# Optimization experiments

Measured on AMD Instinct MI355X. Metric: run time of the kernel, lower is better.

Reference implementation:

```python
import jax, jax.numpy as jnp
import numpy as np

B, D, C, N = 8, 49, 512, 12
BN_EPS = 1e-5
SCALE = (C // 2) ** -0.5


def bn_train(x, axes):
    # training-mode batchnorm, gamma=1 beta=0 (per bn_init / default init)
    m = jnp.mean(x, axis=axes, keepdims=True)
    v = jnp.var(x, axis=axes, keepdims=True)
    return (x - m) * jax.lax.rsqrt(v + BN_EPS)


def l2norm(x):
    n = jnp.linalg.norm(x, axis=-1, keepdims=True)
    return x / jnp.maximum(n, 1e-12)


def cross_attn(y, xkv, wq, bq, wk, bk, wv, bv):
    q = y @ wq + bq
    k = xkv @ wk + bk
    v = xkv @ wv + bv
    a = jax.nn.softmax(jnp.einsum('...ik,...jk->...ij', q, k) * SCALE, axis=-1)
    return a @ v


def _gnn_layer(xv, ed, wa, wb, we, wu, wv):
    # incidence-matrix einsums reduce to repeat (end-gather) / tile (start-gather)
    res = xv
    agg = jnp.repeat(xv @ wa, N, axis=1) + jnp.tile(xv @ wb, (1, N, 1)) + ed @ we
    ed = ed + jax.nn.relu(bn_train(agg, (0, 2)))
    e = jax.nn.sigmoid(ed).reshape(-1, N, N, C)
    e = jax.nn.softmax(e, axis=2).reshape(-1, N * N, C)
    uj = jnp.tile(xv @ wv, (1, N, 1))
    msg = (e * uj).reshape(-1, N, N, C).sum(axis=2) / N  # scatter via end.T
    xv = jax.nn.relu(res + bn_train(xv @ wu + msg, (0, 2)))
    return xv, ed


def setup_inputs() -> dict:
    ks = iter(jax.random.split(jax.random.key(0), 64))

    def nrm(shape, scale=0.02):
        return jax.random.normal(next(ks), shape, dtype=jnp.float32) * scale

    g = float(np.sqrt(2.0 / C))
    inp = {'x': jax.random.normal(next(ks), (B, D, C), dtype=jnp.float32)}
    inp['Wc'] = nrm((N, C, C))
    inp['bc'] = nrm((N, C), 0.01)
    for p in ('fam', 'arm'):
        inp[p + '_wq'] = nrm((C, C // 2))
        inp[p + '_bq'] = nrm((C // 2,), 0.01)
        inp[p + '_wk'] = nrm((C, C // 2))
        inp[p + '_bk'] = nrm((C // 2,), 0.01)
        inp[p + '_wv'] = nrm((C, C))
        inp[p + '_bv'] = nrm((C,), 0.01)
    inp['ep_w'] = nrm((C, C))
    inp['ep_b'] = nrm((C,), 0.01)
    for nm in ('g_wa1', 'g_wb1', 'g_we1', 'g_wu1', 'g_wv1',
               'g_wa2', 'g_wb2', 'g_we2', 'g_wu2', 'g_wv2'):
        inp[nm] = nrm((C, C), g)
    inp['sc'] = nrm((N, C), float(np.sqrt(6.0 / (N + C))))
    inp['efc_w'] = nrm((C, 4), float(np.sqrt(6.0 / (C + 4))))
    inp['efc_b'] = nrm((4,), 0.01)
    return inp


def reference(x, Wc, bc,
              fam_wq, fam_bq, fam_wk, fam_bk, fam_wv, fam_bv,
              arm_wq, arm_bq, arm_wk, arm_bk, arm_wv, arm_bv,
              ep_w, ep_b,
              g_wa1, g_wb1, g_we1, g_wu1, g_wv1,
              g_wa2, g_wb2, g_we2, g_wu2, g_wv2,
              sc, efc_w, efc_b):
    b = x.shape[0]
    # per-class LinearBlocks (fc -> BN -> ReLU), vectorized over classes
    h = jnp.einsum('bdc,nco->bndo', x, Wc) + bc[None, :, None, :]
    f_u = jax.nn.relu(bn_train(h, (0, 2)))          # (b, N, D, C)
    f_v = f_u.mean(axis=2)                           # (b, N, C)
    # GEM edge extractor
    gf = jnp.broadcast_to(x[:, None], (b, N, D, C))
    feat = cross_attn(f_u, gf, fam_wq, fam_bq, fam_wk, fam_bk, fam_wv, fam_bv)
    feat_end = jnp.repeat(feat, N, axis=1)           # (b, N*N, D, C): edge (i,j) -> node i
    feat_start = jnp.tile(feat, (1, N, 1, 1))        # edge (i,j) -> node j
    feat = cross_attn(feat_start, feat_end, arm_wq, arm_bq, arm_wk, arm_bk, arm_wv, arm_bv)
    f_e = bn_train(feat @ ep_w + ep_b, (0, 2, 3)).mean(axis=2)  # (b, N*N, C)
    # cosine-similarity adjacency mask (detached), digraph-normalized
    si = l2norm(jax.lax.stop_gradient(f_v))
    adj = jnp.einsum('bik,bjk->bij', si, si)
    dis = jnp.sum(adj, axis=-1) ** -0.5
    mask = (adj * dis[:, :, None] * dis[:, None, :]).reshape(b, N * N, 1)
    f_e = f_e * mask
    # two GNN message-passing layers
    f_v, f_e = _gnn_layer(f_v, f_e, g_wa1, g_wb1, g_we1, g_wu1, g_wv1)
    f_v, f_e = _gnn_layer(f_v, f_e, g_wa2, g_wb2, g_we2, g_wu2, g_wv2)
    # cosine classifier + edge fc
    scn = l2norm(jax.nn.relu(sc))
    cl = jnp.sum(l2norm(f_v) * scn[None], axis=-1)   # (b, N)
    cl_edge = f_e @ efc_w + efc_b                    # (b, N*N, 4)
    return cl, cl_edge
```

## Files before the change

### kernel.cpp

```cpp
#include <hip/hip_runtime.h>
#include <math.h>

namespace {

constexpr int B = 8, D = 49, C = 512, N = 12, H = 256, E = 144;
constexpr int M_BD  = B * D;
constexpr int M_BND = B * N * D;
constexpr float BN_EPS = 1e-5f;
constexpr float ATT_SCALE = 0.0625f;

typedef __attribute__((ext_vector_type(4))) float  floatx4;
typedef __attribute__((ext_vector_type(8))) short  shortx8;

__device__ inline unsigned short f2bf(float f) {
  unsigned u = __float_as_uint(f);
  return (unsigned short)((u + 0x7fffu + ((u >> 16) & 1u)) >> 16);
}
__device__ inline float bf2f(unsigned short u) {
  return __uint_as_float(((unsigned)u) << 16);
}

__device__ inline void gload16(const unsigned short* g, unsigned short* l) {
  __builtin_amdgcn_global_load_lds(
      (const __attribute__((address_space(1))) void*)g,
      (__attribute__((address_space(3))) void*)l, 16, 0, 0);
}

struct TCJobs {
  const float* src[28];
  unsigned short* dst[28];
  int nn[28];
};

__global__ __launch_bounds__(256)
void tcast_k(TCJobs jobs,
             const float* __restrict__ x, unsigned short* __restrict__ xb,
             const float* __restrict__ awv, unsigned short* __restrict__ armwvb,
             const float* __restrict__ bk, const float* __restrict__ bv,
             const float* __restrict__ bq2, const float* __restrict__ bk2,
             const float* __restrict__ arm_bv, const float* __restrict__ epw,
             const float* __restrict__ epb,
             float* __restrict__ kvbias, float* __restrict__ qkvbias)
{
  const int z = blockIdx.z;
  const int tid = threadIdx.x;
  if (z == 28) {
    int idx = (blockIdx.y * 16 + blockIdx.x) * 256 + tid;
    const int n1 = M_BD * C / 8;
    const int n2 = n1 + C * C / 8;
    if (idx < n1) {
      int i8 = idx * 8;
      float4 a = *reinterpret_cast<const float4*>(x + i8);
      float4 b = *reinterpret_cast<const float4*>(x + i8 + 4);
      shortx8 o;
      o[0]=(short)f2bf(a.x); o[1]=(short)f2bf(a.y); o[2]=(short)f2bf(a.z); o[3]=(short)f2bf(a.w);
      o[4]=(short)f2bf(b.x); o[5]=(short)f2bf(b.y); o[6]=(short)f2bf(b.z); o[7]=(short)f2bf(b.w);
      *reinterpret_cast<shortx8*>(xb + i8) = o;
    } else if (idx < n2) {
      int i8 = (idx - n1) * 8;
      float4 a = *reinterpret_cast<const float4*>(awv + i8);
      float4 b = *reinterpret_cast<const float4*>(awv + i8 + 4);
      shortx8 o;
      o[0]=(short)f2bf(a.x); o[1]=(short)f2bf(a.y); o[2]=(short)f2bf(a.z); o[3]=(short)f2bf(a.w);
      o[4]=(short)f2bf(b.x); o[5]=(short)f2bf(b.y); o[6]=(short)f2bf(b.z); o[7]=(short)f2bf(b.w);
      *reinterpret_cast<shortx8*>(armwvb + i8) = o;
    } else if (idx >= 58112 && idx < 58624) {
      int c = idx - 58112;
      float s = epb[c];
      for (int k = 0; k < C; ++k) s = fmaf(arm_bv[k], epw[k * C + c], s);
      qkvbias[512 + c] = s;
    }
    if (idx < 256) { kvbias[idx] = bk[idx]; qkvbias[idx] = bq2[idx]; qkvbias[256 + idx] = bk2[idx]; }
    if (idx < 512) kvbias[256 + idx] = bv[idx];
    return;
  }
  const float* src = jobs.src[z];
  unsigned short* dst = jobs.dst[z];
  const int Nn = jobs.nn[z];
  const int tx = blockIdx.x, ty = blockIdx.y;
  if (tx * 32 >= Nn) return;
  __shared__ float t[32][33];
  const int lr = tid >> 5, lc = tid & 31;
#pragma unroll
  for (int p = 0; p < 4; ++p) {
    int k = ty * 32 + p * 8 + lr;
    t[p * 8 + lr][lc] = src[(long long)k * Nn + tx * 32 + lc];
  }
  __syncthreads();
#pragma unroll
  for (int p = 0; p < 4; ++p) {
    int n = tx * 32 + p * 8 + lr;
    dst[(long long)n * 512 + ty * 32 + lc] = f2bf(t[lc][p * 8 + lr]);
  }
}

__device__ __forceinline__
void gemm64_body(const void* __restrict__ Ain, const unsigned short* __restrict__ Bt,
                 const float* __restrict__ bp, float* __restrict__ co,
                 unsigned short* __restrict__ cb,
                 int M, int Nn, int K, int lda, int ldb, int ldc, int abf,
                 int bx, int by)
{
  const float* Af = abf ? nullptr : (const float*)Ain;
  const unsigned short* Ab = abf ? (const unsigned short*)Ain : nullptr;

  __shared__ short As[64 * 72];
  __shared__ short Bs[64 * 72];

  const int tid = threadIdx.x;
  const int row0 = bx * 64, col0 = by * 64;
  const int wid = tid >> 6, lane = tid & 63;
  const int wr = wid >> 1, wc = wid & 1;
  const int lr = lane & 15, lg = lane >> 4;

  floatx4 acc00 = {0.f,0.f,0.f,0.f}, acc01 = {0.f,0.f,0.f,0.f};
  floatx4 acc10 = {0.f,0.f,0.f,0.f}, acc11 = {0.f,0.f,0.f,0.f};

  const int r = tid >> 2, seg = tid & 3;
  const int gr = row0 + r, gn = col0 + r;
  short* aw = &As[r * 72 + seg * 16];
  short* bw = &Bs[r * 72 + seg * 16];
  const shortx8 zz = {0,0,0,0,0,0,0,0};

  for (int k0 = 0; k0 < K; k0 += 64) {
    shortx8 w0, w1;
    if (gr < M) {
      if (abf) {
        const shortx8* ap = reinterpret_cast<const shortx8*>(Ab + (long long)gr * lda + seg * 16 + k0);
        w0 = ap[0]; w1 = ap[1];
      } else {
        const float4* ap = reinterpret_cast<const float4*>(Af + (long long)gr * lda + seg * 16 + k0);
        float4 fa0 = ap[0], fa1 = ap[1], fa2 = ap[2], fa3 = ap[3];
        w0[0]=(short)f2bf(fa0.x); w0[1]=(short)f2bf(fa0.y); w0[2]=(short)f2bf(fa0.z); w0[3]=(short)f2bf(fa0.w);
        w0[4]=(short)f2bf(fa1.x); w0[5]=(short)f2bf(fa1.y); w0[6]=(short)f2bf(fa1.z); w0[7]=(short)f2bf(fa1.w);
        w1[0]=(short)f2bf(fa2.x); w1[1]=(short)f2bf(fa2.y); w1[2]=(short)f2bf(fa2.z); w1[3]=(short)f2bf(fa2.w);
        w1[4]=(short)f2bf(fa3.x); w1[5]=(short)f2bf(fa3.y); w1[6]=(short)f2bf(fa3.z); w1[7]=(short)f2bf(fa3.w);
      }
    } else { w0 = zz; w1 = zz; }
    const shortx8* bp8 = reinterpret_cast<const shortx8*>(Bt + (long long)gn * ldb + seg * 16 + k0);
    shortx8 b0v = bp8[0];
    shortx8 b1v = bp8[1];

    __syncthreads();
    *reinterpret_cast<shortx8*>(aw)     = w0;
    *reinterpret_cast<shortx8*>(aw + 8) = w1;
    *reinterpret_cast<shortx8*>(bw)     = b0v;
    *reinterpret_cast<shortx8*>(bw + 8) = b1v;
    __syncthreads();

#pragma unroll
    for (int kt = 0; kt < 2; ++kt) {
      shortx8 a0 = *reinterpret_cast<const shortx8*>(&As[(wr*32      + lr) * 72 + kt*32 + lg*8]);
      shortx8 a1 = *reinterpret_cast<const shortx8*>(&As[(wr*32 + 16 + lr) * 72 + kt*32 + lg*8]);
      shortx8 bb0 = *reinterpret_cast<const shortx8*>(&Bs[(wc*32      + lr) * 72 + kt*32 + lg*8]);
      shortx8 bb1 = *reinterpret_cast<const shortx8*>(&Bs[(wc*32 + 16 + lr) * 72 + kt*32 + lg*8]);
      acc00 = __builtin_amdgcn_mfma_f32_16x16x32_bf16(a0, bb0, acc00, 0, 0, 0);
      acc01 = __builtin_amdgcn_mfma_f32_16x16x32_bf16(a0, bb1, acc01, 0, 0, 0);
      acc10 = __builtin_amdgcn_mfma_f32_16x16x32_bf16(a1, bb0, acc10, 0, 0, 0);
      acc11 = __builtin_amdgcn_mfma_f32_16x16x32_bf16(a1, bb1, acc11, 0, 0, 0);
    }
  }

  const int colA = col0 + wc * 32 + lr;
  const int colB = colA + 16;
  const bool okA = colA < Nn, okB = colB < Nn;
  const float biasA = (bp && okA) ? bp[colA] : 0.f;
  const float biasB = (bp && okB) ? bp[colB] : 0.f;
  const int rb0 = row0 + wr * 32 + lg * 4;
  const int rb1 = rb0 + 16;
#pragma unroll
  for (int jj = 0; jj < 4; ++jj) {
    int ra = rb0 + jj, rb = rb1 + jj;
    float v00 = acc00[jj] + biasA, v01 = acc01[jj] + biasB;
    float v10 = acc10[jj] + biasA, v11 = acc11[jj] + biasB;
    if (ra < M) {
      if (co) { if (okA) co[(long long)ra * ldc + colA] = v00;
                if (okB) co[(long long)ra * ldc + colB] = v01; }
      if (cb) { if (okA) cb[(long long)ra * ldc + colA] = f2bf(v00);
                if (okB) cb[(long long)ra * ldc + colB] = f2bf(v01); }
    }
    if (rb < M) {
      if (co) { if (okA) co[(long long)rb * ldc + colA] = v10;
                if (okB) co[(long long)rb * ldc + colB] = v11; }
      if (cb) { if (okA) cb[(long long)rb * ldc + colA] = f2bf(v10);
                if (okB) cb[(long long)rb * ldc + colB] = f2bf(v11); }
    }
  }
}

__global__ __launch_bounds__(256)
void gemm_mfma(const void* __restrict__ Ain, const unsigned short* __restrict__ Bt,
               const float* __restrict__ bias, float* __restrict__ Co,
               unsigned short* __restrict__ Cb,
               int M, int Nn, int K, int lda, int ldb, int ldc, int abf,
               long long sA, long long sB, long long sBias, long long sC)
{
  const int z = blockIdx.z;
  const void* A = abf ? (const void*)((const unsigned short*)Ain + z * sA)
                      : (const void*)((const float*)Ain + z * sA);
  gemm64_body(A, Bt + z * sB, bias ? bias + z * sBias : nullptr,
              Co ? Co + z * sC : nullptr, Cb ? Cb + z * sC : nullptr,
              M, Nn, K, lda, ldb, ldc, abf, blockIdx.x, blockIdx.y);
}

struct GJob {
  const void* A; const unsigned short* B; const float* bias;
  float* Co; unsigned short* Cb;
  int M, Nn, K, lda, ldb, ldc, abf, tx;
};
struct GJobs { GJob j[3]; int ends[3]; int n; };

__global__ __launch_bounds__(256)
void gemm_jobs(GJobs js)
{
  const int bid = blockIdx.x;
#pragma unroll
  for (int q = 0; q < 3; ++q) {
    if (q < js.n && bid < js.ends[q]) {
      int start = q ? js.ends[q - 1] : 0;
      int local = bid - start;
      const GJob& J = js.j[q];
      gemm64_body(J.A, J.B, J.bias, J.Co, J.Cb,
                  J.M, J.Nn, J.K, J.lda, J.ldb, J.ldc, J.abf,
                  local % J.tx, local / J.tx);
      return;
    }
  }
}

__device__ __forceinline__
void g128_body(const unsigned short* __restrict__ Ab, const unsigned short* __restrict__ Bt,
               const float* __restrict__ bp, float* __restrict__ co,
               unsigned short* __restrict__ cb, float* __restrict__ psb, float* __restrict__ pqb,
               int M, int Nn, int K, int lda, int ldb, int ldc, int bx, int by)
{
  __shared__ unsigned short As[128 * 64];
  __shared__ unsigned short Bs[128 * 64];

  const int tid = threadIdx.x;
  const int row0 = bx * 128, col0 = by * 128;
  const int wid = tid >> 6, lane = tid & 63;
  const int wr = wid >> 1, wc = wid & 1;
  const int lr = lane & 15, lg = lane >> 4;

  floatx4 acc[4][4];
#pragma unroll
  for (int mf = 0; mf < 4; ++mf)
#pragma unroll
    for (int nf = 0; nf < 4; ++nf) acc[mf][nf] = floatx4{0.f,0.f,0.f,0.f};

  const int rsub = tid >> 3;
  const int csub = (tid & 7) * 8;

  for (int k0 = 0; k0 < K; k0 += 64) {
    __syncthreads();
#pragma unroll
    for (int it = 0; it < 4; ++it) {
      int r = it * 32 + rsub;
      gload16(Ab + (long long)(row0 + r) * lda + k0 + csub, As + it * 2048 + tid * 8);
      gload16(Bt + (long long)(col0 + r) * ldb + k0 + csub, Bs + it * 2048 + tid * 8);
    }
    __syncthreads();

#pragma unroll
    for (int kt = 0; kt < 2; ++kt) {
      shortx8 af[4], bf[4];
#pragma unroll
      for (int mf = 0; mf < 4; ++mf)
        af[mf] = *reinterpret_cast<const shortx8*>(&As[(wr*64 + mf*16 + lr) * 64 + kt*32 + lg*8]);
#pragma unroll
      for (int nf = 0; nf < 4; ++nf)
        bf[nf] = *reinterpret_cast<const shortx8*>(&Bs[(wc*64 + nf*16 + lr) * 64 + kt*32 + lg*8]);
#pragma unroll
      for (int mf = 0; mf < 4; ++mf)
#pragma unroll
        for (int nf = 0; nf < 4; ++nf)
          acc[mf][nf] = __builtin_amdgcn_mfma_f32_16x16x32_bf16(af[mf], bf[nf], acc[mf][nf], 0, 0, 0);
    }
  }

#pragma unroll
  for (int nf = 0; nf < 4; ++nf) {
    const int col = col0 + wc * 64 + nf * 16 + lr;
    if (col >= Nn) continue;
    const float bv = bp ? bp[col] : 0.f;
#pragma unroll
    for (int mf = 0; mf < 4; ++mf) {
      const int rbase = row0 + wr * 64 + mf * 16 + lg * 4;
#pragma unroll
      for (int jj = 0; jj < 4; ++jj) {
        int row = rbase + jj;
        if (row >= M) continue;
        float v = acc[mf][nf][jj] + bv;
        if (co) co[(long long)row * ldc + col] = v;
        if (cb) cb[(long long)row * ldc + col] = f2bf(v);
      }
    }
  }

  if (psb) {
    __syncthreads();
    float* sb = (float*)As;
    sb[tid] = 0.f;
    __syncthreads();
#pragma unroll
    for (int nf = 0; nf < 4; ++nf) {
      const int lcol = wc * 64 + nf * 16 + lr;
      const int col = col0 + lcol;
      float s = 0.f, q = 0.f;
      if (col < Nn) {
        const float bv = bp ? bp[col] : 0.f;
#pragma unroll
        for (int mf = 0; mf < 4; ++mf) {
          const int rbase = row0 + wr * 64 + mf * 16 + lg * 4;
#pragma unroll
          for (int jj = 0; jj < 4; ++jj) {
            if (rbase + jj < M) { float v = acc[mf][nf][jj] + bv; s += v; q += v * v; }
          }
        }
      }
      atomicAdd(&sb[lcol], s);
      atomicAdd(&sb[128 + lcol], q);
    }
    __syncthreads();
    if (tid < 128) {
      psb[col0 + tid] = sb[tid];
      pqb[col0 + tid] = sb[128 + tid];
    }
  }
}

__global__ __launch_bounds__(256)
void gemm128g(const unsigned short* __restrict__ Ab, const unsigned short* __restrict__ Bt,
              const float* __restrict__ bias, float* __restrict__ Co,
              unsigned short* __restrict__ Cb, float* __restrict__ ps, float* __restrict__ pq,
              int M, int Nn, int K, int lda, int ldb, int ldc,
              long long sA, long long sB, long long sBias, long long sC)
{
  const int z = blockIdx.z;
  long long so = ((long long)blockIdx.x * gridDim.z + z) * ldc;
  g128_body(Ab + z * sA, Bt + z * sB, bias ? bias + z * sBias : nullptr,
            Co ? Co + z * sC : nullptr, Cb ? Cb + z * sC : nullptr,
            ps ? ps + so : nullptr, pq ? pq + so : nullptr,
            M, Nn, K, lda, ldb, ldc, blockIdx.x, blockIdx.y);
}

__global__ __launch_bounds__(256)
void scgm_k(const unsigned short* __restrict__ qkvfe, float* __restrict__ Sc,
            float* __restrict__ Gm)
{
  const int bid = blockIdx.x;
  if (bid < 200) {
    int z = bid / 25, rem = bid % 25;
    g128_body(qkvfe + (long long)z * 588 * 1024, qkvfe + 256 + (long long)z * 588 * 1024,
              nullptr, Sc + (long long)z * 588 * 588, nullptr, nullptr, nullptr,
              588, 588, H, 1024, 1024, 588, rem % 5, rem / 5);
  } else {
    int z = bid - 200;
    const unsigned short* vp = qkvfe + 512 + (long long)z * 49 * 1024;
    gemm64_body(vp, vp, nullptr, Gm + (long long)z * 2401, nullptr,
                D, D, C, 1024, 1024, D, 1, 0, 0);
  }
}

__global__ __launch_bounds__(256)
void gnn_gemm_k(const unsigned short* __restrict__ feb, const unsigned short* __restrict__ wet,
                float* __restrict__ EW, const float* __restrict__ fv,
                const unsigned short* __restrict__ ABUVt, float* __restrict__ ABUV)
{
  const int bid = blockIdx.x;
  if (bid < 36) {
    g128_body(feb, wet, nullptr, EW, nullptr, nullptr, nullptr,
              B * E, C, C, C, C, C, bid % 9, bid / 9);
  } else {
    int local = bid - 36;
    gemm64_body(fv, ABUVt, nullptr, ABUV, nullptr,
                B * N, 2048, C, C, C, 2048, 0, local % 2, local / 2);
  }
}

__global__ __launch_bounds__(256)
void fu_fv(const unsigned short* __restrict__ hb, const float* __restrict__ ps,
           const float* __restrict__ pq, unsigned short* __restrict__ fub,
           float* __restrict__ fv)
{
  const int bid = blockIdx.x;
  const int b = bid / N, n = bid % N;
  const int c = blockIdx.y * 256 + threadIdx.x;
  const int idx = n * C + c;
  float s = 0.f, q = 0.f;
#pragma unroll
  for (int sl = 0; sl < 4; ++sl) { s += ps[sl * (N * C) + idx]; q += pq[sl * (N * C) + idx]; }
  float m = s / (float)M_BD;
  float rv = rsqrtf(q / (float)M_BD - m * m + BN_EPS);
  float acc = 0.f;
  for (int d = 0; d < D; ++d) {
    float v = bf2f(hb[((long long)n * M_BD + b * D + d) * C + c]);
    v = fmaxf((v - m) * rv, 0.f);
    fub[((long long)bid * D + d) * C + c] = f2bf(v);
    acc += v;
  }
  fv[(long long)bid * C + c] = acc * (1.0f / (float)D);
}

__global__ __launch_bounds__(256)
void softvxt_k(const float* __restrict__ Sf, unsigned short* __restrict__ Ppb,
               const unsigned short* __restrict__ kvx, unsigned short* __restrict__ vxtb,
               const float* __restrict__ fv, float* __restrict__ maskp)
{
  const int tid = threadIdx.x;
  if (blockIdx.x < 19) {
    int row = blockIdx.x * 256 + tid;
    if (row >= M_BND) return;
    const float* p = Sf + (long long)row * 49;
    float v[49];
    float m = -1e30f;
#pragma unroll
    for (int j = 0; j < 49; ++j) { v[j] = p[j] * ATT_SCALE; m = fmaxf(m, v[j]); }
    float s = 0.f;
#pragma unroll
    for (int j = 0; j < 49; ++j) { v[j] = __expf(v[j] - m); s += v[j]; }
    float inv = 1.f / s;
    unsigned short* o = Ppb + (long long)row * 64;
#pragma unroll
    for (int j = 0; j < 49; ++j) o[j] = f2bf(v[j] * inv);
#pragma unroll
    for (int j = 49; j < 64; ++j) o[j] = 0;
    return;
  }
  if (blockIdx.x < 83) {
    const int i = blockIdx.x - 19;
    const int b = i >> 3, cc = i & 7;
    __shared__ unsigned short t[49][65];
    for (int idx = tid; idx < 49 * 64; idx += 256) {
      int rr = idx >> 6, k = idx & 63;
      t[rr][k] = kvx[(long long)(b * 49 + rr) * 768 + 256 + cc * 64 + k];
    }
    __syncthreads();
    for (int idx = tid; idx < 64 * 64; idx += 256) {
      int n = idx >> 6, kk = idx & 63;
      vxtb[((long long)b * 512 + cc * 64 + n) * 64 + kk] = (kk < 49) ? t[kk][n] : (unsigned short)0;
    }
    return;
  }
  const int b = blockIdx.x - 83;
  __shared__ float fl[N][C];
  __shared__ float adj[N][N];
  __shared__ float nrm[N];
  __shared__ float dis[N];
  for (int idx = tid; idx < N * C; idx += 256)
    fl[idx / C][idx % C] = fv[(long long)b * N * C + idx];
  __syncthreads();
  if (tid < N * N) {
    int i = tid / N, j = tid % N;
    float s = 0.f;
    for (int k = 0; k < C; ++k) s += fl[i][k] * fl[j][k];
    adj[i][j] = s;
  }
  __syncthreads();
  if (tid < N) nrm[tid] = fmaxf(sqrtf(adj[tid][tid]), 1e-12f);
  __syncthreads();
  if (tid < N * N) {
    int i = tid / N, j = tid % N;
    adj[i][j] = adj[i][j] / (nrm[i] * nrm[j]);
  }
  __syncthreads();
  if (tid < N) {
    float s = 0.f;
    for (int j = 0; j < N; ++j) s += adj[tid][j];
    dis[tid] = rsqrtf(s);
  }
  __syncthreads();
  if (tid < N * N) {
    int i = tid / N, j = tid % N;
    maskp[b * E + tid] = adj[i][j] * dis[i] * dis[j];
  }
}

__global__ __launch_bounds__(256)
void edge_finish(const float* __restrict__ Sc, const float* __restrict__ G,
                 const unsigned short* __restrict__ qkvfe,
                 float* __restrict__ S1, float* __restrict__ eS)
{
  const int bid = blockIdx.x;
  const int b = bid / E, e = bid % E;
  const int i = e / N, j = e % N;
  const float* Scb = Sc + (long long)b * 588 * 588 + (long long)(j * 49) * 588 + i * 49;
  const float* Gp  = G + (long long)(b * N + i) * 2401;
  const unsigned short* Vp = qkvfe + (long long)(b * N + i) * D * 1024 + 512;

  __shared__ float aT[49][53];
  __shared__ float g[49][53];
  __shared__ unsigned short abT[64][72];
  __shared__ float ws[52];
  __shared__ float r0[4], r1[4];
  const int tid = threadIdx.x;
  const int wid = tid >> 6, lane = tid & 63;
  const int lr = lane & 15, lg = lane >> 4;

  for (int idx = tid; idx < 49 * 49; idx += 256) {
    int di = idx / 49, dj = idx - di * 49;
    aT[dj][di] = Scb[di * 588 + dj] * ATT_SCALE;
    g[di][dj] = Gp[idx];
  }
  __syncthreads();
  if (tid < D) {
    float m = -1e30f;
    for (int jj = 0; jj < D; ++jj) m = fmaxf(m, aT[jj][tid]);
    float s = 0.f;
    for (int jj = 0; jj < D; ++jj) { float ev = __expf(aT[jj][tid] - m); aT[jj][tid] = ev; s += ev; }
    float inv = 1.f / s;
    for (int jj = 0; jj < D; ++jj) aT[jj][tid] *= inv;
  }
  __syncthreads();
  for (int idx = tid; idx < 64 * 64; idx += 256) {
    int dj = idx >> 6, di = idx & 63;
    float v = (dj < D && di < D) ? aT[dj][di] : 0.f;
    abT[dj][di] = f2bf(v);
  }
  if (tid < D) {
    float s = 0.f;
    for (int di = 0; di < D; ++di) s += aT[tid][di];
    ws[tid] = s;
  }
  __syncthreads();

  floatx4 acc[4];
#pragma unroll
  for (int tk = 0; tk < 4; ++tk) acc[tk] = floatx4{0.f,0.f,0.f,0.f};
  shortx8 af0 = *reinterpret_cast<const shortx8*>(&abT[wid * 16 + lr][lg * 8]);
  shortx8 af1 = *reinterpret_cast<const shortx8*>(&abT[wid * 16 + lr][32 + lg * 8]);
#pragma unroll
  for (int tk = 0; tk < 4; ++tk) {
    shortx8 bf0v = *reinterpret_cast<const shortx8*>(&abT[tk * 16 + lr][lg * 8]);
    shortx8 bf1v = *reinterpret_cast<const shortx8*>(&abT[tk * 16 + lr][32 + lg * 8]);
    acc[tk] = __builtin_amdgcn_mfma_f32_16x16x32_bf16(af0, bf0v, acc[tk], 0, 0, 0);
    acc[tk] = __builtin_amdgcn_mfma_f32_16x16x32_bf16(af1, bf1v, acc[tk], 0, 0, 0);
  }
  float st2 = 0.f;
#pragma unroll
  for (int tk = 0; tk < 4; ++tk) {
    int kcol = tk * 16 + lr;
#pragma unroll
    for (int rg = 0; rg < 4; ++rg) {
      int jrow = wid * 16 + lg * 4 + rg;
      if (jrow < D && kcol < D) st2 = fmaf(acc[tk][rg], g[jrow][kcol], st2);
    }
  }

  const unsigned* Vp32 = reinterpret_cast<const unsigned*>(Vp);
  float s1a = 0.f, s1b = 0.f;
  for (int dk = 0; dk < D; ++dk) {
    unsigned u = Vp32[dk * 512 + tid];
    float w = ws[dk];
    s1a = fmaf(w, bf2f((unsigned short)(u & 0xffffu)), s1a);
    s1b = fmaf(w, bf2f((unsigned short)(u >> 16)), s1b);
  }
  S1[(long long)bid * C + 2 * tid]     = s1a;
  S1[(long long)bid * C + 2 * tid + 1] = s1b;
  float st = s1a + s1b;

  for (int off = 32; off; off >>= 1) { st += __shfl_down(st, off); st2 += __shfl_down(st2, off); }
  if (lane == 0) { r0[wid] = st; r1[wid] = st2; }
  __syncthreads();
  if (tid == 0) {
    eS[bid * 2 + 0] = r0[0] + r0[1] + r0[2] + r0[3];
    eS[bid * 2 + 1] = r1[0] + r1[1] + r1[2] + r1[3];
  }
}

__global__ __launch_bounds__(256)
void fe_k(const float* __restrict__ S1, const float* __restrict__ eS,
          const float* __restrict__ maskp, float* __restrict__ fe,
          unsigned short* __restrict__ feb)
{
  __shared__ float csh[3];
  long long idx0 = (long long)blockIdx.x * 256;
  long long be = idx0 / C;
  int e = (int)(be % E);
  if (threadIdx.x == 0) {
    float s = 0.f, q = 0.f;
    for (int b = 0; b < B; ++b) { s += eS[(b * E + e) * 2]; q += eS[(b * E + e) * 2 + 1]; }
    const float inv = 1.f / (float)(B * D * C);
    float m = s * inv;
    csh[0] = m;
    csh[1] = rsqrtf(q * inv - m * m + BN_EPS);
    csh[2] = maskp[be];
  }
  __syncthreads();
  long long idx = idx0 + threadIdx.x;
  float v = (S1[idx] * (1.0f / (float)D) - csh[0]) * csh[1] * csh[2];
  fe[idx] = v;
  feb[idx] = f2bf(v);
}

__global__ __launch_bounds__(256)
void agg_stats(const float* __restrict__ ABUV, const float* __restrict__ EW,
               float* __restrict__ mu_e, float* __restrict__ rs_e)
{
  const int e = blockIdx.x;
  const int i = e / N, j = e % N;
  const int tid = threadIdx.x;
  float s = 0.f, q = 0.f;
  for (int idx = tid; idx < B * C; idx += 256) {
    int b = idx >> 9, c = idx & 511;
    float v = ABUV[(long long)(b * N + i) * 2048 + c]
            + ABUV[(long long)(b * N + j) * 2048 + 512 + c]
            + EW[((long long)b * E + e) * C + c];
    s += v; q += v * v;
  }
  for (int off = 32; off; off >>= 1) { s += __shfl_down(s, off); q += __shfl_down(q, off); }
  __shared__ float r0[4], r1[4];
  int wid = tid >> 6, lane = tid & 63;
  if (lane == 0) { r0[wid] = s; r1[wid] = q; }
  __syncthreads();
  if (tid == 0) {
    float ss = r0[0] + r0[1] + r0[2] + r0[3];
    float qq = r1[0] + r1[1] + r1[2] + r1[3];
    float m = ss / (float)(B * C);
    mu_e[e] = m;
    rs_e[e] = rsqrtf(qq / (float)(B * C) - m * m + BN_EPS);
  }
}

__global__ __launch_bounds__(256)
void edmsg_k(float* __restrict__ fe, unsigned short* __restrict__ feb,
             const float* __restrict__ ABUV,
             const float* __restrict__ EW, const float* __restrict__ mu_e,
             const float* __restrict__ rs_e, float* __restrict__ pre,
             float* __restrict__ nps, float* __restrict__ npq)
{
  const int bid = blockIdx.x;
  const int b = bid / N, i = bid % N;
  const int tid = threadIdx.x;
  float ls = 0.f, lq = 0.f;
  for (int c = tid; c < C; c += 256) {
    float ai = ABUV[(long long)(b * N + i) * 2048 + c];
    float sv[N];
    float m = -1e30f;
#pragma unroll
    for (int jn = 0; jn < N; ++jn) {
      int e = i * N + jn;
      float v = ai + ABUV[(long long)(b * N + jn) * 2048 + 512 + c]
              + EW[((long long)b * E + e) * C + c];
      v = (v - mu_e[e]) * rs_e[e];
      long long fidx = ((long long)b * E + e) * C + c;
      float ed = fe[fidx] + fmaxf(v, 0.f);
      fe[fidx] = ed;
      feb[fidx] = f2bf(ed);
      float sg = 1.f / (1.f + __expf(-ed));
      sv[jn] = sg; m = fmaxf(m, sg);
    }
    float sum = 0.f;
#pragma unroll
    for (int jn = 0; jn < N; ++jn) { float ev = __expf(sv[jn] - m); sv[jn] = ev; sum += ev; }
    float acc = 0.f;
#pragma unroll
    for (int jn = 0; jn < N; ++jn)
      acc = fmaf(sv[jn], ABUV[(long long)(b * N + jn) * 2048 + 1536 + c], acc);
    acc /= (sum * (float)N);
    float pv = ABUV[(long long)bid * 2048 + 1024 + c] + acc;
    pre[(long long)bid * C + c] = pv;
    ls += pv; lq += pv * pv;
  }
  for (int off = 32; off; off >>= 1) { ls += __shfl_down(ls, off); lq += __shfl_down(lq, off); }
  __shared__ float r0[4], r1[4];
  int wid = tid >> 6, lane = tid & 63;
  if (lane == 0) { r0[wid] = ls; r1[wid] = lq; }
  __syncthreads();
  if (tid == 0) {
    nps[i * B + b] = r0[0] + r0[1] + r0[2] + r0[3];
    npq[i * B + b] = r1[0] + r1[1] + r1[2] + r1[3];
  }
}

__global__ void xv_update(float* __restrict__ xv, const float* __restrict__ pre,
                          const float* __restrict__ nps, const float* __restrict__ npq)
{
  long long idx = (long long)blockIdx.x * 256 + threadIdx.x;
  if (idx >= (long long)B * N * C) return;
  int i = (int)((idx / C) % N);
  float s = 0.f, q = 0.f;
#pragma unroll
  for (int bb = 0; bb < B; ++bb) { s += nps[i * B + bb]; q += npq[i * B + bb]; }
  float mu = s * (1.f / (float)(B * C));
  float rs = rsqrtf(q * (1.f / (float)(B * C)) - mu * mu + BN_EPS);
  float v = xv[idx] + (pre[idx] - mu) * rs;
  xv[idx] = fmaxf(v, 0.f);
}

__global__ __launch_bounds__(256)
void out_k(const float* __restrict__ xv, const float* __restrict__ sc,
           const float* __restrict__ ed, const float* __restrict__ w,
           const float* __restrict__ bias, float* __restrict__ out)
{
  const int bid = blockIdx.x;
  const int tid = threadIdx.x;
  int wid = tid >> 6, lane = tid & 63;
  if (bid < B * N) {
    const int b = bid / N, i = bid % N;
    float sxx = 0.f, sss = 0.f, sxs = 0.f;
    for (int c = tid; c < C; c += 256) {
      float xvv = xv[(long long)(b * N + i) * C + c];
      float scv = fmaxf(sc[i * C + c], 0.f);
      sxx += xvv * xvv; sss += scv * scv; sxs += xvv * scv;
    }
    for (int off = 32; off; off >>= 1) {
      sxx += __shfl_down(sxx, off);
      sss += __shfl_down(sss, off);
      sxs += __shfl_down(sxs, off);
    }
    __shared__ float r0[4], r1[4], r2[4];
    if (lane == 0) { r0[wid] = sxx; r1[wid] = sss; r2[wid] = sxs; }
    __syncthreads();
    if (tid == 0) {
      float a = r0[0] + r0[1] + r0[2] + r0[3];
      float s = r1[0] + r1[1] + r1[2] + r1[3];
      float p = r2[0] + r2[1] + r2[2] + r2[3];
      float nx = fmaxf(sqrtf(a), 1e-12f);
      float ns = fmaxf(sqrtf(s), 1e-12f);
      out[b * N + i] = p / (nx * ns);
    }
  } else {
    const int eb = bid - B * N;
    float a0 = 0, a1 = 0, a2 = 0, a3 = 0;
    for (int c = tid; c < C; c += 256) {
      float v = ed[(long long)eb * C + c];
      a0 = fmaf(v, w[c * 4 + 0], a0);
      a1 = fmaf(v, w[c * 4 + 1], a1);
      a2 = fmaf(v, w[c * 4 + 2], a2);
      a3 = fmaf(v, w[c * 4 + 3], a3);
    }
    for (int off = 32; off; off >>= 1) {
      a0 += __shfl_down(a0, off);
      a1 += __shfl_down(a1, off);
      a2 += __shfl_down(a2, off);
      a3 += __shfl_down(a3, off);
    }
    __shared__ float r[4][4];
    if (lane == 0) { r[wid][0] = a0; r[wid][1] = a1; r[wid][2] = a2; r[wid][3] = a3; }
    __syncthreads();
    if (tid < 4) {
      float s = r[0][tid] + r[1][tid] + r[2][tid] + r[3][tid];
      out[B * N + eb * 4 + tid] = s + bias[tid];
    }
  }
}

}

extern "C" void kernel_launch(void* const* d_in, const int* in_sizes, int n_in,
                              void* d_out, int out_size, void* d_ws, size_t ws_size,
                              hipStream_t stream)
{
  (void)in_sizes; (void)n_in; (void)out_size; (void)ws_size;
  const float* x      = (const float*)d_in[0];
  const float* Wc     = (const float*)d_in[1];
  const float* bc     = (const float*)d_in[2];
  const float* fam_wq = (const float*)d_in[3];
  const float* fam_bq = (const float*)d_in[4];
  const float* fam_wk = (const float*)d_in[5];
  const float* fam_bk = (const float*)d_in[6];
  const float* fam_wv = (const float*)d_in[7];
  const float* fam_bv = (const float*)d_in[8];
  const float* arm_wq = (const float*)d_in[9];
  const float* arm_bq = (const float*)d_in[10];
  const float* arm_wk = (const float*)d_in[11];
  const float* arm_bk = (const float*)d_in[12];
  const float* arm_wv = (const float*)d_in[13];
  const float* arm_bv = (const float*)d_in[14];
  const float* ep_w   = (const float*)d_in[15];
  const float* ep_b   = (const float*)d_in[16];
  const float* gw[10] = {
    (const float*)d_in[17], (const float*)d_in[18], (const float*)d_in[19],
    (const float*)d_in[20], (const float*)d_in[21],
    (const float*)d_in[22], (const float*)d_in[23], (const float*)d_in[24],
    (const float*)d_in[25], (const float*)d_in[26]};
  const float* sc     = (const float*)d_in[27];
  const float* efc_w  = (const float*)d_in[28];
  const float* efc_b  = (const float*)d_in[29];
  float* out = (float*)d_out;

  char* wsb = (char*)d_ws;
  size_t off = 0;
  auto allocf = [&](size_t n) { float* p = (float*)(wsb + off); off += ((n * 4 + 255) / 256) * 256; return p; };
  auto allocu = [&](size_t n) { unsigned short* p = (unsigned short*)(wsb + off); off += ((n * 2 + 255) / 256) * 256; return p; };

  float* Sc    = allocf(2766336);
  float* bnp_s = allocf(24576);
  float* bnp_q = allocf(24576);
  float* f_v   = allocf(49152);
  float* Sf    = allocf(230496);
  float* Gm    = allocf(230496);
  float* S1    = allocf(589824);
  float* fe    = allocf(589824);
  float* EW    = allocf(589824);
  float* eS    = allocf(2304);
  float* mask  = allocf(1152);
  float* ABUV  = allocf(196608);
  float* pre   = allocf(49152);
  float* mu_e  = allocf(144);
  float* rs_e  = allocf(144);
  float* nps   = allocf(96);
  float* npq   = allocf(96);
  float* kvbias  = allocf(768);
  float* qkvbias = allocf(1024);

  unsigned short* Wct    = allocu(3145728);
  unsigned short* famqt  = allocu(131072);
  unsigned short* kvwt   = allocu(393216);
  unsigned short* qkw2t  = allocu(524288);
  unsigned short* epwt   = allocu(262144);
  unsigned short* armwvb = allocu(262144);
  unsigned short* wet0   = allocu(262144);
  unsigned short* wet1   = allocu(262144);
  unsigned short* ABUVt0 = allocu(1048576);
  unsigned short* ABUVt1 = allocu(1048576);
  unsigned short* xb     = allocu(262144);
  unsigned short* hb     = allocu(2408448);
  unsigned short* fub    = allocu(2408448);
  unsigned short* q1b    = allocu(1204224);
  unsigned short* kxvx_b = allocu(350208);
  unsigned short* Ppb    = allocu(301056);
  unsigned short* vxtb   = allocu(262144);
  unsigned short* featb  = allocu(2424832);
  unsigned short* qkvfe  = allocu(4915200);
  unsigned short* feb    = allocu(589824);

  dim3 blk(256);

  TCJobs tj{};
  int jn = 0;
  for (int n = 0; n < 12; ++n) { tj.src[jn] = Wc + (size_t)n * C * C; tj.dst[jn] = Wct + (size_t)n * C * C; tj.nn[jn] = C; ++jn; }
  tj.src[jn] = fam_wq; tj.dst[jn] = famqt;             tj.nn[jn] = H; ++jn;
  tj.src[jn] = fam_wk; tj.dst[jn] = kvwt;              tj.nn[jn] = H; ++jn;
  tj.src[jn] = fam_wv; tj.dst[jn] = kvwt + 256 * 512;  tj.nn[jn] = C; ++jn;
  tj.src[jn] = arm_wq; tj.dst[jn] = qkw2t;             tj.nn[jn] = H; ++jn;
  tj.src[jn] = arm_wk; tj.dst[jn] = qkw2t + 256 * 512; tj.nn[jn] = H; ++jn;
  tj.src[jn] = ep_w;   tj.dst[jn] = epwt;              tj.nn[jn] = C; ++jn;
  tj.src[jn] = gw[2];  tj.dst[jn] = wet0;              tj.nn[jn] = C; ++jn;
  tj.src[jn] = gw[7];  tj.dst[jn] = wet1;              tj.nn[jn] = C; ++jn;
  tj.src[jn] = gw[0];  tj.dst[jn] = ABUVt0;               tj.nn[jn] = C; ++jn;
  tj.src[jn] = gw[1];  tj.dst[jn] = ABUVt0 + 1 * C * C;   tj.nn[jn] = C; ++jn;
  tj.src[jn] = gw[3];  tj.dst[jn] = ABUVt0 + 2 * C * C;   tj.nn[jn] = C; ++jn;
  tj.src[jn] = gw[4];  tj.dst[jn] = ABUVt0 + 3 * C * C;   tj.nn[jn] = C; ++jn;
  tj.src[jn] = gw[5];  tj.dst[jn] = ABUVt1;               tj.nn[jn] = C; ++jn;
  tj.src[jn] = gw[6];  tj.dst[jn] = ABUVt1 + 1 * C * C;   tj.nn[jn] = C; ++jn;
  tj.src[jn] = gw[8];  tj.dst[jn] = ABUVt1 + 2 * C * C;   tj.nn[jn] = C; ++jn;
  tj.src[jn] = gw[9];  tj.dst[jn] = ABUVt1 + 3 * C * C;   tj.nn[jn] = C; ++jn;
  tcast_k<<<dim3(16, 16, 29), blk, 0, stream>>>(tj, x, xb, arm_wv, armwvb,
      fam_bk, fam_bv, arm_bq, arm_bk, arm_bv, ep_w, ep_b, kvbias, qkvbias);

  gemm128g<<<dim3(4, 4, 12), blk, 0, stream>>>(xb, Wct, bc, nullptr, hb, bnp_s, bnp_q,
      M_BD, C, C, C, C, C, 0LL, (long long)C * C, (long long)C, (long long)M_BD * C);
  fu_fv<<<dim3(B * N, 2), blk, 0, stream>>>(hb, bnp_s, bnp_q, fub, f_v);

  {
    GJobs js{};
    js.j[0] = {fub,  famqt,  fam_bq, nullptr, q1b,            M_BND, H,   C, C, C, H,   1, 74};
    js.j[1] = {xb,   kvwt,   kvbias, nullptr, kxvx_b,         M_BD,  768, C, C, C, 768, 1, 7};
    js.j[2] = {epwt, armwvb, nullptr, nullptr, qkw2t + 512 * 512, C,  C,   C, C, C, C,   1, 8};
    js.ends[0] = 296; js.ends[1] = 380; js.ends[2] = 444; js.n = 3;
    gemm_jobs<<<dim3(444), blk, 0, stream>>>(js);
  }
  gemm_mfma<<<dim3(10, 1, 8), blk, 0, stream>>>(q1b, kxvx_b, nullptr, Sf, nullptr,
      588, 49, H, H, 768, 49, 1, 588LL * 256, 49LL * 768, 0LL, 588LL * 49);
  softvxt_k<<<dim3(91), blk, 0, stream>>>(Sf, Ppb, kxvx_b, vxtb, f_v, mask);
  gemm_mfma<<<dim3(10, 8, 8), blk, 0, stream>>>(Ppb, vxtb, nullptr, nullptr, featb,
      588, C, 64, 64, 64, C, 1, 588LL * 64, 512LL * 64, 0LL, 588LL * 512);

  gemm128g<<<dim3(37, 8, 1), blk, 0, stream>>>(featb, qkw2t, qkvbias, nullptr, qkvfe,
      nullptr, nullptr, M_BND, 1024, C, C, C, 1024, 0, 0, 0, 0);

  scgm_k<<<dim3(296), blk, 0, stream>>>(qkvfe, Sc, Gm);

  edge_finish<<<dim3(B * E), blk, 0, stream>>>(Sc, Gm, qkvfe, S1, eS);
  fe_k<<<dim3(2304), blk, 0, stream>>>(S1, eS, mask, fe, feb);

  for (int L = 0; L < 2; ++L) {
    const unsigned short* ABUVt = L ? ABUVt1 : ABUVt0;
    const unsigned short* wet   = L ? wet1 : wet0;
    gnn_gemm_k<<<dim3(100), blk, 0, stream>>>(feb, wet, EW, f_v, ABUVt, ABUV);
    agg_stats<<<dim3(E), blk, 0, stream>>>(ABUV, EW, mu_e, rs_e);
    edmsg_k<<<dim3(B * N), blk, 0, stream>>>(fe, feb, ABUV, EW, mu_e, rs_e, pre, nps, npq);
    xv_update<<<dim3((B * N * C + 255) / 256), blk, 0, stream>>>(f_v, pre, nps, npq);
  }

  out_k<<<dim3(B * N + B * E), blk, 0, stream>>>(f_v, sc, fe, efc_w, efc_b, out);
}
```

Measured before the change: 213.7 us.

## Regroup projection GEMMs, store attention scores in bf16, fuse final node update

Merges the per-class projection GEMM with the kv and ep-weight GEMMs into one launch, and gives the fam query projection its own launch, which cuts kernel count and regroups independent work. The arm-attention score matrix and the Gram matrix are now written and read as bf16 instead of fp32, halving that intermediate traffic. The second layer's xv_update is folded into out_k, which recomputes the batchnorm, residual and relu inline. The bf16 scores add rounding before softmax, and the fu_fv dependency now waits on a larger combined kernel.

```diff
diff --git a/kernel.cpp b/kernel.cpp
--- a/kernel.cpp
+++ b/kernel.cpp
@@ -203,31 +203,6 @@
               M, Nn, K, lda, ldb, ldc, abf, blockIdx.x, blockIdx.y);
 }
 
-struct GJob {
-  const void* A; const unsigned short* B; const float* bias;
-  float* Co; unsigned short* Cb;
-  int M, Nn, K, lda, ldb, ldc, abf, tx;
-};
-struct GJobs { GJob j[3]; int ends[3]; int n; };
-
-__global__ __launch_bounds__(256)
-void gemm_jobs(GJobs js)
-{
-  const int bid = blockIdx.x;
-#pragma unroll
-  for (int q = 0; q < 3; ++q) {
-    if (q < js.n && bid < js.ends[q]) {
-      int start = q ? js.ends[q - 1] : 0;
-      int local = bid - start;
-      const GJob& J = js.j[q];
-      gemm64_body(J.A, J.B, J.bias, J.Co, J.Cb,
-                  J.M, J.Nn, J.K, J.lda, J.ldb, J.ldc, J.abf,
-                  local % J.tx, local / J.tx);
-      return;
-    }
-  }
-}
-
 __device__ __forceinline__
 void g128_body(const unsigned short* __restrict__ Ab, const unsigned short* __restrict__ Bt,
                const float* __restrict__ bp, float* __restrict__ co,
@@ -346,36 +321,48 @@
 }
 
 __global__ __launch_bounds__(256)
-void scgm_k(const unsigned short* __restrict__ qkvfe, float* __restrict__ Sc,
-            float* __restrict__ Gm)
+void proj1_k(const unsigned short* __restrict__ xb, const unsigned short* __restrict__ Wct,
+             const float* __restrict__ bc, unsigned short* __restrict__ hb,
+             float* __restrict__ ps, float* __restrict__ pq,
+             const unsigned short* __restrict__ kvwt, const float* __restrict__ kvbias,
+             unsigned short* __restrict__ kxvx_b,
+             const unsigned short* __restrict__ epwt, const unsigned short* __restrict__ armwvb,
+             unsigned short* __restrict__ w2out)
+{
+  const int bid = blockIdx.x;
+  if (bid < 192) {
+    int z = bid >> 4, rem = bid & 15;
+    int bx = rem & 3, by = rem >> 2;
+    long long so = ((long long)bx * 12 + z) * C;
+    g128_body(xb, Wct + (long long)z * C * C, bc + (long long)z * C,
+              nullptr, hb + (long long)z * M_BD * C, ps + so, pq + so,
+              M_BD, C, C, C, C, C, bx, by);
+  } else if (bid < 276) {
+    int local = bid - 192;
+    gemm64_body(xb, kvwt, kvbias, nullptr, kxvx_b, M_BD, 768, C, C, C, 768, 1,
+                local % 7, local / 7);
+  } else {
+    int local = bid - 276;
+    gemm64_body(epwt, armwvb, nullptr, nullptr, w2out, C, C, C, C, C, C, 1,
+                local % 8, local / 8);
+  }
+}
+
+__global__ __launch_bounds__(256)
+void scgm_k(const unsigned short* __restrict__ qkvfe, unsigned short* __restrict__ Sc16,
+            unsigned short* __restrict__ Gm16)
 {
   const int bid = blockIdx.x;
   if (bid < 200) {
     int z = bid / 25, rem = bid % 25;
     g128_body(qkvfe + (long long)z * 588 * 1024, qkvfe + 256 + (long long)z * 588 * 1024,
-              nullptr, Sc + (long long)z * 588 * 588, nullptr, nullptr, nullptr,
+              nullptr, nullptr, Sc16 + (long long)z * 588 * 588, nullptr, nullptr,
               588, 588, H, 1024, 1024, 588, rem % 5, rem / 5);
   } else {
     int z = bid - 200;
     const unsigned short* vp = qkvfe + 512 + (long long)z * 49 * 1024;
-    gemm64_body(vp, vp, nullptr, Gm + (long long)z * 2401, nullptr,
+    gemm64_body(vp, vp, nullptr, nullptr, Gm16 + (long long)z * 2401,
                 D, D, C, 1024, 1024, D, 1, 0, 0);
-  }
-}
-
-__global__ __launch_bounds__(256)
-void gnn_gemm_k(const unsigned short* __restrict__ feb, const unsigned short* __restrict__ wet,
-                float* __restrict__ EW, const float* __restrict__ fv,
-                const unsigned short* __restrict__ ABUVt, float* __restrict__ ABUV)
-{
-  const int bid = blockIdx.x;
-  if (bid < 36) {
-    g128_body(feb, wet, nullptr, EW, nullptr, nullptr, nullptr,
-              B * E, C, C, C, C, C, bid % 9, bid / 9);
-  } else {
-    int local = bid - 36;
-    gemm64_body(fv, ABUVt, nullptr, ABUV, nullptr,
-                B * N, 2048, C, C, C, 2048, 0, local % 2, local / 2);
   }
 }
 
@@ -478,15 +465,15 @@
 }
 
 __global__ __launch_bounds__(256)
-void edge_finish(const float* __restrict__ Sc, const float* __restrict__ G,
+void edge_finish(const unsigned short* __restrict__ Sc16, const unsigned short* __restrict__ G16,
                  const unsigned short* __restrict__ qkvfe,
                  float* __restrict__ S1, float* __restrict__ eS)
 {
   const int bid = blockIdx.x;
   const int b = bid / E, e = bid % E;
   const int i = e / N, j = e % N;
-  const float* Scb = Sc + (long long)b * 588 * 588 + (long long)(j * 49) * 588 + i * 49;
-  const float* Gp  = G + (long long)(b * N + i) * 2401;
+  const unsigned short* Scb = Sc16 + (long long)b * 588 * 588 + (long long)(j * 49) * 588 + i * 49;
+  const unsigned short* Gp  = G16 + (long long)(b * N + i) * 2401;
   const unsigned short* Vp = qkvfe + (long long)(b * N + i) * D * 1024 + 512;
 
   __shared__ float aT[49][53];
@@ -500,8 +487,8 @@
 
   for (int idx = tid; idx < 49 * 49; idx += 256) {
     int di = idx / 49, dj = idx - di * 49;
-    aT[dj][di] = Scb[di * 588 + dj] * ATT_SCALE;
-    g[di][dj] = Gp[idx];
+    aT[dj][di] = bf2f(Scb[di * 588 + dj]) * ATT_SCALE;
+    g[di][dj] = bf2f(Gp[idx]);
   }
   __syncthreads();
   if (tid < D) {
@@ -595,6 +582,22 @@
 }
 
 __global__ __launch_bounds__(256)
+void gnn_gemm_k(const unsigned short* __restrict__ feb, const unsigned short* __restrict__ wet,
+                float* __restrict__ EW, const float* __restrict__ fv,
+                const unsigned short* __restrict__ ABUVt, float* __restrict__ ABUV)
+{
+  const int bid = blockIdx.x;
+  if (bid < 36) {
+    g128_body(feb, wet, nullptr, EW, nullptr, nullptr, nullptr,
+              B * E, C, C, C, C, C, bid % 9, bid / 9);
+  } else {
+    int local = bid - 36;
+    gemm64_body(fv, ABUVt, nullptr, ABUV, nullptr,
+                B * N, 2048, C, C, C, 2048, 0, local % 2, local / 2);
+  }
+}
+
+__global__ __launch_bounds__(256)
 void agg_stats(const float* __restrict__ ABUV, const float* __restrict__ EW,
                float* __restrict__ mu_e, float* __restrict__ rs_e)
 {
@@ -690,7 +693,9 @@
 }
 
 __global__ __launch_bounds__(256)
-void out_k(const float* __restrict__ xv, const float* __restrict__ sc,
+void out_k(const float* __restrict__ xv, const float* __restrict__ pre,
+           const float* __restrict__ nps, const float* __restrict__ npq,
+           const float* __restrict__ sc,
            const float* __restrict__ ed, const float* __restrict__ w,
            const float* __restrict__ bias, float* __restrict__ out)
 {
@@ -699,9 +704,14 @@
   int wid = tid >> 6, lane = tid & 63;
   if (bid < B * N) {
     const int b = bid / N, i = bid % N;
+    float s = 0.f, q = 0.f;
+#pragma unroll
+    for (int t = 0; t < B; ++t) { s += nps[i * B + t]; q += npq[i * B + t]; }
+    float mu = s * (1.f / (float)(B * C));
+    float rs = rsqrtf(q * (1.f / (float)(B * C)) - mu * mu + BN_EPS);
     float sxx = 0.f, sss = 0.f, sxs = 0.f;
     for (int c = tid; c < C; c += 256) {
-      float xvv = xv[(long long)(b * N + i) * C + c];
+      float xvv = fmaxf(xv[(long long)bid * C + c] + (pre[(long long)bid * C + c] - mu) * rs, 0.f);
       float scv = fmaxf(sc[i * C + c], 0.f);
       sxx += xvv * xvv; sss += scv * scv; sxs += xvv * scv;
     }
@@ -715,10 +725,10 @@
     __syncthreads();
     if (tid == 0) {
       float a = r0[0] + r0[1] + r0[2] + r0[3];
-      float s = r1[0] + r1[1] + r1[2] + r1[3];
+      float ss = r1[0] + r1[1] + r1[2] + r1[3];
       float p = r2[0] + r2[1] + r2[2] + r2[3];
       float nx = fmaxf(sqrtf(a), 1e-12f);
-      float ns = fmaxf(sqrtf(s), 1e-12f);
+      float ns = fmaxf(sqrtf(ss), 1e-12f);
       out[b * N + i] = p / (nx * ns);
     }
   } else {
@@ -741,8 +751,8 @@
     if (lane == 0) { r[wid][0] = a0; r[wid][1] = a1; r[wid][2] = a2; r[wid][3] = a3; }
     __syncthreads();
     if (tid < 4) {
-      float s = r[0][tid] + r[1][tid] + r[2][tid] + r[3][tid];
-      out[B * N + eb * 4 + tid] = s + bias[tid];
+      float sr = r[0][tid] + r[1][tid] + r[2][tid] + r[3][tid];
+      out[B * N + eb * 4 + tid] = sr + bias[tid];
     }
   }
 }
@@ -786,12 +796,10 @@
   auto allocf = [&](size_t n) { float* p = (float*)(wsb + off); off += ((n * 4 + 255) / 256) * 256; return p; };
   auto allocu = [&](size_t n) { unsigned short* p = (unsigned short*)(wsb + off); off += ((n * 2 + 255) / 256) * 256; return p; };
 
-  float* Sc    = allocf(2766336);
   float* bnp_s = allocf(24576);
   float* bnp_q = allocf(24576);
   float* f_v   = allocf(49152);
   float* Sf    = allocf(230496);
-  float* Gm    = allocf(230496);
   float* S1    = allocf(589824);
   float* fe    = allocf(589824);
   float* EW    = allocf(589824);
@@ -826,6 +834,8 @@
   unsigned short* featb  = allocu(2424832);
   unsigned short* qkvfe  = allocu(4915200);
   unsigned short* feb    = allocu(589824);
+  unsigned short* Sc16   = allocu(2765952);
+  unsigned short* Gm16   = allocu(230496);
 
   dim3 blk(256);
 
@@ -851,18 +861,12 @@
   tcast_k<<<dim3(16, 16, 29), blk, 0, stream>>>(tj, x, xb, arm_wv, armwvb,
       fam_bk, fam_bv, arm_bq, arm_bk, arm_bv, ep_w, ep_b, kvbias, qkvbias);
 
-  gemm128g<<<dim3(4, 4, 12), blk, 0, stream>>>(xb, Wct, bc, nullptr, hb, bnp_s, bnp_q,
-      M_BD, C, C, C, C, C, 0LL, (long long)C * C, (long long)C, (long long)M_BD * C);
+  proj1_k<<<dim3(340), blk, 0, stream>>>(xb, Wct, bc, hb, bnp_s, bnp_q,
+      kvwt, kvbias, kxvx_b, epwt, armwvb, qkw2t + 512 * 512);
   fu_fv<<<dim3(B * N, 2), blk, 0, stream>>>(hb, bnp_s, bnp_q, fub, f_v);
 
-  {
-    GJobs js{};
-    js.j[0] = {fub,  famqt,  fam_bq, nullptr, q1b,            M_BND, H,   C, C, C, H,   1, 74};
-    js.j[1] = {xb,   kvwt,   kvbias, nullptr, kxvx_b,         M_BD,  768, C, C, C, 768, 1, 7};
-    js.j[2] = {epwt, armwvb, nullptr, nullptr, qkw2t + 512 * 512, C,  C,   C, C, C, C,   1, 8};
-    js.ends[0] = 296; js.ends[1] = 380; js.ends[2] = 444; js.n = 3;
-    gemm_jobs<<<dim3(444), blk, 0, stream>>>(js);
-  }
+  gemm_mfma<<<dim3(74, 4, 1), blk, 0, stream>>>(fub, famqt, fam_bq, nullptr, q1b,
+      M_BND, H, C, C, C, H, 1, 0, 0, 0, 0);
   gemm_mfma<<<dim3(10, 1, 8), blk, 0, stream>>>(q1b, kxvx_b, nullptr, Sf, nullptr,
       588, 49, H, H, 768, 49, 1, 588LL * 256, 49LL * 768, 0LL, 588LL * 49);
   softvxt_k<<<dim3(91), blk, 0, stream>>>(Sf, Ppb, kxvx_b, vxtb, f_v, mask);
@@ -872,9 +876,9 @@
   gemm128g<<<dim3(37, 8, 1), blk, 0, stream>>>(featb, qkw2t, qkvbias, nullptr, qkvfe,
       nullptr, nullptr, M_BND, 1024, C, C, C, 1024, 0, 0, 0, 0);
 
-  scgm_k<<<dim3(296), blk, 0, stream>>>(qkvfe, Sc, Gm);
-
-  edge_finish<<<dim3(B * E), blk, 0, stream>>>(Sc, Gm, qkvfe, S1, eS);
+  scgm_k<<<dim3(296), blk, 0, stream>>>(qkvfe, Sc16, Gm16);
+
+  edge_finish<<<dim3(B * E), blk, 0, stream>>>(Sc16, Gm16, qkvfe, S1, eS);
   fe_k<<<dim3(2304), blk, 0, stream>>>(S1, eS, mask, fe, feb);
 
   for (int L = 0; L < 2; ++L) {
@@ -883,8 +887,9 @@
     gnn_gemm_k<<<dim3(100), blk, 0, stream>>>(feb, wet, EW, f_v, ABUVt, ABUV);
     agg_stats<<<dim3(E), blk, 0, stream>>>(ABUV, EW, mu_e, rs_e);
     edmsg_k<<<dim3(B * N), blk, 0, stream>>>(fe, feb, ABUV, EW, mu_e, rs_e, pre, nps, npq);
-    xv_update<<<dim3((B * N * C + 255) / 256), blk, 0, stream>>>(f_v, pre, nps, npq);
-  }
-
-  out_k<<<dim3(B * N + B * E), blk, 0, stream>>>(f_v, sc, fe, efc_w, efc_b, out);
-}
+    if (L == 0)
+      xv_update<<<dim3((B * N * C + 255) / 256), blk, 0, stream>>>(f_v, pre, nps, npq);
+  }
+
+  out_k<<<dim3(B * N + B * E), blk, 0, stream>>>(f_v, pre, nps, npq, sc, fe, efc_w, efc_b, out);
+}
```

Measured after the change: 209.6 us. About the same (-1.9%).
